# Kernel tuning notes

Measured on AMD Instinct MI355X. Metric: run time of the kernel, lower is better.

## Reference

```python
import jax, jax.numpy as jnp
import numpy as np

N = 100_000   # nodes
E = 1_600_000 # edges (avg degree 16)
D = 128       # input_dim
H = 128       # hidden_dim
G = 64        # graphs in batch
C = 2         # num_classes


def setup_inputs() -> dict:
    key = jax.random.key(0)
    ks = jax.random.split(key, 16)
    x = jax.random.normal(ks[0], (N, D), dtype=jnp.float32)
    edge_index = jax.random.randint(ks[1], (2, E), 0, N, dtype=jnp.int32)
    batch = jnp.sort(jax.random.randint(ks[2], (N,), 0, G, dtype=jnp.int32))
    def lin(k, fin, fout):
        s = 1.0 / np.sqrt(fin)
        kw, kb = jax.random.split(k)
        W = jax.random.uniform(kw, (fin, fout), jnp.float32, -s, s)
        b = jax.random.uniform(kb, (fout,), jnp.float32, -s, s)
        return W, b
    W0, b0 = lin(ks[3], D, H)
    W1, b1 = lin(ks[4], H, H)
    W2, b2 = lin(ks[5], H, H)
    Wc1, bc1 = lin(ks[6], 2 * H, H)
    Wc2, bc2 = lin(ks[7], H, C)
    return dict(x=x, edge_index=edge_index, batch=batch,
                W0=W0, b0=b0, W1=W1, b1=b1, W2=W2, b2=b2,
                Wc1=Wc1, bc1=bc1, Wc2=Wc2, bc2=bc2)


def _gcn_layer(x, W, b, src, dst, dinv):
    # GCNConv with self-loops and symmetric normalization:
    # out_i = sum_{j->i} d_j^{-1/2} d_i^{-1/2} (x_j W) + d_i^{-1} (x_i W) + b
    h = x @ W                                   # [N, H]
    coef = dinv[src] * dinv[dst]                # [E]
    agg = jax.ops.segment_sum(h[src] * coef[:, None], dst, num_segments=N)
    return agg + h * (dinv * dinv)[:, None] + b


def reference(x, edge_index, batch, W0, b0, W1, b1, W2, b2, Wc1, bc1, Wc2, bc2):
    src, dst = edge_index[0], edge_index[1]
    # degree with self-loops (in-degree on target nodes + 1)
    deg = jax.ops.segment_sum(jnp.ones((E,), jnp.float32), dst, num_segments=N) + 1.0
    dinv = jax.lax.rsqrt(deg)
    for W, b in ((W0, b0), (W1, b1), (W2, b2)):
        x = jax.nn.relu(_gcn_layer(x, W, b, src, dst, dinv))
        # dropout: inference mode -> identity
    # global mean pool per graph
    sums = jax.ops.segment_sum(x, batch, num_segments=G)            # [G, H]
    cnt = jax.ops.segment_sum(jnp.ones((N,), jnp.float32), batch, num_segments=G)
    pooled = sums / jnp.maximum(cnt, 1.0)[:, None]
    combined = jnp.concatenate([pooled, pooled], axis=1)            # [G, 2H]
    hcls = jax.nn.relu(combined @ Wc1 + bc1)
    return hcls @ Wc2 + bc2                                         # [G, C]
```

## Files before the change

kernel.cpp:

```cpp
#include <hip/hip_runtime.h>

#define HDIM 128
#define GCOUNT 64
#define CHUNK 2048

__device__ __forceinline__ float bfl(unsigned u) { return __uint_as_float(u << 16); }
__device__ __forceinline__ float bfh(unsigned u) { return __uint_as_float(u & 0xffff0000u); }
__device__ __forceinline__ unsigned short f2bf(float f) {
  unsigned u = __float_as_uint(f);
  unsigned r = (u + 0x7fffu + ((u >> 16) & 1u)) >> 16;
  return (unsigned short)r;
}
__device__ __forceinline__ unsigned pk2(float a, float b) {
  return (unsigned)f2bf(a) | ((unsigned)f2bf(b) << 16);
}

typedef __attribute__((ext_vector_type(8))) short short8;
typedef __attribute__((ext_vector_type(4))) float f32x4;

__device__ __forceinline__ unsigned qb(float v, float rinv) {
  int q = (int)rintf(v * rinv);
  return (unsigned)(q & 0xff);
}


__global__ void mega1(const float* __restrict__ W0, const float* __restrict__ W1,
                      const float* __restrict__ W2,
                      unsigned short* __restrict__ h0, unsigned short* __restrict__ l0,
                      unsigned short* __restrict__ h1, unsigned short* __restrict__ l1,
                      unsigned short* __restrict__ h2, unsigned short* __restrict__ l2,
                      float* __restrict__ pooled, float* __restrict__ gcnt, int pz,
                      const int* __restrict__ dst, int E, int G, int NB1,
                      int* __restrict__ gcount,
                      const float* __restrict__ x, uint2* __restrict__ S,
                      float* __restrict__ cs_base, int n) {
  __shared__ int hist[512];
  int b = blockIdx.x, t = threadIdx.x;
  if (b < 192) {
    int w = b >> 6;
    int idx = (b & 63) * 256 + t;
    const float* W = (w == 0) ? W0 : (w == 1) ? W1 : W2;
    unsigned short* hi = (w == 0) ? h0 : (w == 1) ? h1 : h2;
    unsigned short* lo = (w == 0) ? l0 : (w == 1) ? l1 : l2;
    int k = idx >> 7, nn = idx & 127;
    float wv = W[idx];
    unsigned short h = f2bf(wv);
    float hf = __uint_as_float((unsigned)h << 16);
    unsigned short l = f2bf(wv - hf);
    int kb = k >> 5, quad = (k >> 3) & 3, e = k & 7;
    int nt = nn >> 4, m = nn & 15;
    int di = (((kb * 8 + nt) * 64) + quad * 16 + m) * 8 + e;
    hi[di] = h;
    lo[di] = l;
  } else if (b < 192 + pz) {
    int i = (b - 192) * 256 + t;
    if (i < GCOUNT * HDIM) pooled[i] = 0.f;
    else if (i - GCOUNT * HDIM < GCOUNT) gcnt[i - GCOUNT * HDIM] = 0.f;
  } else if (b < 192 + pz + G) {
    int blk = b - 192 - pz;
    for (int i = t; i < NB1; i += 256) hist[i] = 0;
    __syncthreads();
    int base = blk * CHUNK;
    #pragma unroll
    for (int j = 0; j < CHUNK / 256; j++) {
      int e = base + j * 256 + t;
      if (e < E) atomicAdd(&hist[dst[e] >> 8], 1);
    }
    __syncthreads();
    for (int i = t; i < NB1; i += 256) gcount[i * G + blk] = hist[i];
  } else {
    int idx = (b - 192 - pz - G) * 16 + (t >> 4);
    int l = t & 15;
    int ridx = min(idx, n - 1);
    float4 f0 = ((const float4*)x)[(size_t)ridx * 32 + l * 2];
    float4 f1 = ((const float4*)x)[(size_t)ridx * 32 + l * 2 + 1];
    float v0 = f0.x, v1 = f0.y, v2 = f0.z, v3 = f0.w;
    float v4 = f1.x, v5 = f1.y, v6 = f1.z, v7 = f1.w;
    float mx = fmaxf(fmaxf(fmaxf(fabsf(v0), fabsf(v1)), fmaxf(fabsf(v2), fabsf(v3))),
                     fmaxf(fmaxf(fabsf(v4), fabsf(v5)), fmaxf(fabsf(v6), fabsf(v7))));
    mx = fmaxf(mx, __shfl_xor(mx, 1));
    mx = fmaxf(mx, __shfl_xor(mx, 2));
    mx = fmaxf(mx, __shfl_xor(mx, 4));
    mx = fmaxf(mx, __shfl_xor(mx, 8));
    float c = mx * (1.0f / 127.0f);
    float rinv = (mx > 0.f) ? 127.0f / mx : 0.f;
    if (idx < n) {
      unsigned lo = qb(v0, rinv) | (qb(v1, rinv) << 8) | (qb(v2, rinv) << 16) | (qb(v3, rinv) << 24);
      unsigned hi = qb(v4, rinv) | (qb(v5, rinv) << 8) | (qb(v6, rinv) << 16) | (qb(v7, rinv) << 24);
      S[(size_t)idx * 16 + l] = make_uint2(lo, hi);
      if (l == 0) cs_base[idx] = c;
    }
  }
}


__global__ void scanA(int* __restrict__ g, int* __restrict__ bsum, int M) {
  __shared__ int sh[1024];
  int t = threadIdx.x;
  int i = blockIdx.x * 1024 + t;
  int v = (i < M) ? g[i] : 0;
  sh[t] = v;
  __syncthreads();
  for (int off = 1; off < 1024; off <<= 1) {
    int u = (t >= off) ? sh[t - off] : 0;
    __syncthreads();
    sh[t] += u;
    __syncthreads();
  }
  if (i < M) g[i] = sh[t] - v;
  if (t == 1023) bsum[blockIdx.x] = sh[1023];
}

__global__ void scanB(int* __restrict__ g, const int* __restrict__ bsum, int nb, int M) {
  __shared__ int sh[512];
  int t = threadIdx.x;
  if (t < 512) sh[t] = (t < nb) ? bsum[t] : 0;
  __syncthreads();
  for (int off = 1; off < 512; off <<= 1) {
    int u = (t < 512 && t >= off) ? sh[t - off] : 0;
    __syncthreads();
    if (t < 512) sh[t] += u;
    __syncthreads();
  }
  #pragma unroll
  for (int k = 0; k < 2; k++) {
    int i = blockIdx.x * 2048 + k * 1024 + t;
    if (i < M) {
      int j = i >> 10;
      if (j) g[i] += sh[j - 1];
    }
  }
}


__global__ void rs_scatter(const int* __restrict__ src, const int* __restrict__ dst,
                           const int* __restrict__ gscan, int E, int G, int NB1,
                           uint2* __restrict__ sp) {
  __shared__ int run[512];
  int blk = blockIdx.x, t = threadIdx.x;
  for (int i = t; i < NB1; i += 256) run[i] = gscan[i * G + blk];
  __syncthreads();
  int base = blk * CHUNK;
  #pragma unroll
  for (int j = 0; j < CHUNK / 256; j++) {
    int e = base + j * 256 + t;
    if (e < E) {
      int d = dst[e];
      int pos = atomicAdd(&run[d >> 8], 1);
      sp[pos] = make_uint2((unsigned)d, (unsigned)src[e]);
    }
  }
}


__global__ void csr_fine(const uint2* __restrict__ sp, const int* __restrict__ gscan,
                         int E, int G, int NB1,
                         int* __restrict__ rowp, int* __restrict__ colv,
                         float* __restrict__ dinv, const float* __restrict__ cs_base,
                         float* __restrict__ cs, int n) {
  __shared__ int hist[256];
  __shared__ int scn[256];
  __shared__ int run2[256];
  int hb = blockIdx.x, t = threadIdx.x;
  int O = gscan[hb * G];
  int Oe = (hb == NB1 - 1) ? E : gscan[(hb + 1) * G];
  if (t < 256) hist[t] = 0;
  __syncthreads();
  for (int e = O + t; e < Oe; e += 512) atomicAdd(&hist[sp[e].x & 255], 1);
  __syncthreads();
  int v = 0;
  if (t < 256) { v = hist[t]; scn[t] = v; }
  __syncthreads();
  for (int off = 1; off < 256; off <<= 1) {
    int u = (t < 256 && t >= off) ? scn[t - off] : 0;
    __syncthreads();
    if (t < 256) scn[t] += u;
    __syncthreads();
  }
  if (t < 256) {
    int excl = scn[t] - v;
    run2[t] = O + excl;
    int d = (hb << 8) + t;
    rowp[d] = O + excl;
    if (d < n) {
      float dv = rsqrtf((float)v + 1.0f);
      dinv[d] = dv;
      cs[d] = cs_base[d] * dv;
    }
  }
  if (hb == NB1 - 1 && t == 0) rowp[n] = E;
  __syncthreads();
  for (int e = O + t; e < Oe; e += 512) {
    uint2 p = sp[e];
    int pos = atomicAdd(&run2[p.x & 255], 1);
    colv[pos] = (int)p.y;
  }
}


__device__ __forceinline__ void acc8(uint2 v, float c, float* a) {
  int xx = (int)v.x, yy = (int)v.y;
  a[0] += c * (float)(signed char)(xx);
  a[1] += c * (float)(signed char)(xx >> 8);
  a[2] += c * (float)(signed char)(xx >> 16);
  a[3] += c * (float)(xx >> 24);
  a[4] += c * (float)(signed char)(yy);
  a[5] += c * (float)(signed char)(yy >> 8);
  a[6] += c * (float)(signed char)(yy >> 16);
  a[7] += c * (float)(yy >> 24);
}


__device__ __forceinline__ void agg_phase(
    const uint2* __restrict__ S, const float* __restrict__ cs,
    const float* __restrict__ dinv,
    const int* __restrict__ rowp, const int* __restrict__ col,
    uint4* At, int block0, int t, int n) {
  int grp = t >> 4, gl = t & 15;
  #pragma unroll 1
  for (int k = 0; k < 4; k++) {
    int lrow = grp * 4 + k;
    int g = block0 + lrow;
    uint4 o = make_uint4(0u, 0u, 0u, 0u);
    if (g < n) {
      float a[8];
      {
        uint2 q = S[(size_t)g * 16 + gl];
        float c = cs[g];
        int xx = (int)q.x, yy = (int)q.y;
        a[0] = c * (float)(signed char)(xx);
        a[1] = c * (float)(signed char)(xx >> 8);
        a[2] = c * (float)(signed char)(xx >> 16);
        a[3] = c * (float)(xx >> 24);
        a[4] = c * (float)(signed char)(yy);
        a[5] = c * (float)(signed char)(yy >> 8);
        a[6] = c * (float)(signed char)(yy >> 16);
        a[7] = c * (float)(yy >> 24);
      }
      int e0 = rowp[g], e1 = rowp[g + 1];
      int e = e0;
      for (; e + 7 < e1; e += 8) {
        int s0 = col[e],     s1 = col[e + 1], s2 = col[e + 2], s3 = col[e + 3];
        int s4 = col[e + 4], s5 = col[e + 5], s6 = col[e + 6], s7 = col[e + 7];
        uint2 q0 = S[(size_t)s0 * 16 + gl];
        uint2 q1 = S[(size_t)s1 * 16 + gl];
        uint2 q2 = S[(size_t)s2 * 16 + gl];
        uint2 q3 = S[(size_t)s3 * 16 + gl];
        uint2 q4 = S[(size_t)s4 * 16 + gl];
        uint2 q5 = S[(size_t)s5 * 16 + gl];
        uint2 q6 = S[(size_t)s6 * 16 + gl];
        uint2 q7 = S[(size_t)s7 * 16 + gl];
        float c0 = cs[s0], c1 = cs[s1], c2 = cs[s2], c3 = cs[s3];
        float c4 = cs[s4], c5 = cs[s5], c6 = cs[s6], c7 = cs[s7];
        acc8(q0, c0, a); acc8(q1, c1, a); acc8(q2, c2, a); acc8(q3, c3, a);
        acc8(q4, c4, a); acc8(q5, c5, a); acc8(q6, c6, a); acc8(q7, c7, a);
      }
      for (; e + 3 < e1; e += 4) {
        int s0 = col[e], s1 = col[e + 1], s2 = col[e + 2], s3 = col[e + 3];
        uint2 q0 = S[(size_t)s0 * 16 + gl];
        uint2 q1 = S[(size_t)s1 * 16 + gl];
        uint2 q2 = S[(size_t)s2 * 16 + gl];
        uint2 q3 = S[(size_t)s3 * 16 + gl];
        float c0 = cs[s0], c1 = cs[s1], c2 = cs[s2], c3 = cs[s3];
        acc8(q0, c0, a); acc8(q1, c1, a); acc8(q2, c2, a); acc8(q3, c3, a);
      }
      for (; e < e1; e++) {
        int s = col[e];
        uint2 q = S[(size_t)s * 16 + gl];
        acc8(q, cs[s], a);
      }
      float d = dinv[g];
      o.x = pk2(a[0] * d, a[1] * d);
      o.y = pk2(a[2] * d, a[3] * d);
      o.z = pk2(a[4] * d, a[5] * d);
      o.w = pk2(a[6] * d, a[7] * d);
    }
    At[(gl << 6) + (lrow ^ (gl & 7))] = o;
  }
}

__device__ __forceinline__ void stage16(uint4* Wl, const uint4* __restrict__ WT, int t) {
  #pragma unroll
  for (int i = 0; i < 4; i++) {
    int idx = t + i * 256;
    Wl[idx] = WT[idx];
  }
}

__device__ __forceinline__ void mfma2(const uint4* Wl, const uint4* av, f32x4* acc,
                                      int kbase, int lane) {
  #pragma unroll
  for (int kk = 0; kk < 2; kk++) {
    short8 af = __builtin_bit_cast(short8, av[kbase + kk]);
    #pragma unroll
    for (int nt = 0; nt < 8; nt++) {
      uint4 b = Wl[(kk * 8 + nt) * 64 + lane];
      acc[nt] = __builtin_amdgcn_mfma_f32_16x16x32_bf16(af, __builtin_bit_cast(short8, b), acc[nt], 0, 0, 0);
    }
  }
}

__global__ __launch_bounds__(256, 8) void fused_q8(
    const uint2* __restrict__ S, const float* __restrict__ cs,
    const float* __restrict__ dinv,
    const int* __restrict__ rowp, const int* __restrict__ col,
    const uint4* __restrict__ WThi, const uint4* __restrict__ WTlo,
    const float* __restrict__ bias,
    unsigned char* __restrict__ Sout, float* __restrict__ csout, int n) {
  __shared__ __align__(16) char smem[16384];
  uint4* At = (uint4*)smem;
  uint4* Wl = (uint4*)smem;
  int t = threadIdx.x;
  int lane = t & 63, wv = t >> 6;
  int m = lane & 15, quad = lane >> 4;
  int block0 = blockIdx.x * 64;

  agg_phase(S, cs, dinv, rowp, col, At, block0, t, n);
  __syncthreads();

  uint4 av[4];
  #pragma unroll
  for (int kb = 0; kb < 4; kb++) {
    int glr = kb * 4 + quad;
    av[kb] = At[(glr << 6) + ((wv * 16 + m) ^ (glr & 7))];
  }
  __syncthreads();

  f32x4 acc[8];
  #pragma unroll
  for (int i = 0; i < 8; i++) acc[i] = (f32x4){0.f, 0.f, 0.f, 0.f};

  stage16(Wl, WThi, t);        __syncthreads();
  mfma2(Wl, av, acc, 0, lane); __syncthreads();
  stage16(Wl, WThi + 1024, t); __syncthreads();
  mfma2(Wl, av, acc, 2, lane); __syncthreads();
  stage16(Wl, WTlo, t);        __syncthreads();
  mfma2(Wl, av, acc, 0, lane); __syncthreads();
  stage16(Wl, WTlo + 1024, t); __syncthreads();
  mfma2(Wl, av, acc, 2, lane); __syncthreads();

  char* stg = smem;
  float* LcA = (float*)(smem + 9216);
  #pragma unroll
  for (int r = 0; r < 4; r++) {
    int lrow = wv * 16 + quad * 4 + r;
    int grow = block0 + lrow;
    float sc = (grow < n) ? dinv[grow] : 0.f;
    float v[8];
    float mx = 0.f;
    #pragma unroll
    for (int nt = 0; nt < 8; nt++) {
      v[nt] = fmaxf(acc[nt][r] + bias[nt * 16 + m], 0.f) * sc;
      mx = fmaxf(mx, v[nt]);
    }
    mx = fmaxf(mx, __shfl_xor(mx, 1));
    mx = fmaxf(mx, __shfl_xor(mx, 2));
    mx = fmaxf(mx, __shfl_xor(mx, 4));
    mx = fmaxf(mx, __shfl_xor(mx, 8));
    float c = mx * (1.0f / 127.0f);
    float rinv = (mx > 0.f) ? 127.0f / mx : 0.f;
    #pragma unroll
    for (int nt = 0; nt < 8; nt++) {
      stg[lrow * 144 + nt * 16 + m] = (char)(int)rintf(v[nt] * rinv);
    }
    if (m == 0) LcA[lrow] = c;
  }
  __syncthreads();
  for (int i = t; i < 512; i += 256) {
    int lrow = i >> 3, seg = i & 7;
    int grow = block0 + lrow;
    if (grow < n)
      ((uint4*)Sout)[(size_t)grow * 8 + seg] = *(const uint4*)&stg[lrow * 144 + seg * 16];
  }
  if (t < 64 && block0 + t < n) csout[block0 + t] = LcA[t];
}

__global__ __launch_bounds__(256, 8) void fused_final(
    const uint2* __restrict__ S, const float* __restrict__ cs,
    const float* __restrict__ dinv,
    const int* __restrict__ rowp, const int* __restrict__ col,
    const uint4* __restrict__ WThi, const uint4* __restrict__ WTlo,
    const float* __restrict__ bias, const int* __restrict__ batch,
    float* __restrict__ pooled, float* __restrict__ gcnt, int n) {
  __shared__ __align__(16) char smem[16384];
  uint4* At = (uint4*)smem;
  uint4* Wl = (uint4*)smem;
  int t = threadIdx.x;
  int lane = t & 63, wv = t >> 6;
  int m = lane & 15, quad = lane >> 4;
  int block0 = blockIdx.x * 64;

  agg_phase(S, cs, dinv, rowp, col, At, block0, t, n);
  __syncthreads();

  uint4 av[4];
  #pragma unroll
  for (int kb = 0; kb < 4; kb++) {
    int glr = kb * 4 + quad;
    av[kb] = At[(glr << 6) + ((wv * 16 + m) ^ (glr & 7))];
  }
  __syncthreads();

  f32x4 acc[8];
  #pragma unroll
  for (int i = 0; i < 8; i++) acc[i] = (f32x4){0.f, 0.f, 0.f, 0.f};

  stage16(Wl, WThi, t);        __syncthreads();
  mfma2(Wl, av, acc, 0, lane); __syncthreads();
  stage16(Wl, WThi + 1024, t); __syncthreads();
  mfma2(Wl, av, acc, 2, lane); __syncthreads();
  stage16(Wl, WTlo, t);        __syncthreads();
  mfma2(Wl, av, acc, 0, lane); __syncthreads();
  stage16(Wl, WTlo + 1024, t); __syncthreads();
  mfma2(Wl, av, acc, 2, lane); __syncthreads();

  unsigned short* Ls = (unsigned short*)smem;
  #pragma unroll
  for (int r = 0; r < 4; r++) {
    int lrow = wv * 16 + quad * 4 + r;
    #pragma unroll
    for (int nt = 0; nt < 8; nt++) {
      float v = fmaxf(acc[nt][r] + bias[nt * 16 + m], 0.f);
      Ls[lrow * 128 + nt * 16 + m] = f2bf(v);
    }
  }
  __syncthreads();
  if (t < 128) {
    float a2 = 0.f, cl = 0.f;
    int gcur = -1;
    for (int r = 0; r < 64; r++) {
      int grow = block0 + r;
      if (grow >= n) break;
      int gr = batch[grow];
      if (gr != gcur) {
        if (gcur >= 0) {
          atomicAdd(&pooled[gcur * HDIM + t], a2);
          if (t == 0) atomicAdd(&gcnt[gcur], cl);
        }
        a2 = 0.f; cl = 0.f; gcur = gr;
      }
      a2 += bfl((unsigned)Ls[r * 128 + t]);
      cl += 1.f;
    }
    if (gcur >= 0) {
      atomicAdd(&pooled[gcur * HDIM + t], a2);
      if (t == 0) atomicAdd(&gcnt[gcur], cl);
    }
  }
}


__global__ void cls_kernel(const float* __restrict__ pooled, const float* __restrict__ gcnt,
                           const float* __restrict__ Wc1, const float* __restrict__ bc1,
                           const float* __restrict__ Wc2, const float* __restrict__ bc2,
                           float* __restrict__ out) {
  __shared__ float p[HDIM];
  __shared__ float r0s[HDIM], r1s[HDIM];
  int g = blockIdx.x, t = threadIdx.x;
  float c = fmaxf(gcnt[g], 1.0f);
  p[t] = pooled[g * HDIM + t] / c;
  __syncthreads();
  float acc = bc1[t];
  for (int k = 0; k < HDIM; k++) {
    acc += p[k] * (Wc1[k * HDIM + t] + Wc1[(HDIM + k) * HDIM + t]);
  }
  float h = fmaxf(acc, 0.f);
  r0s[t] = h * Wc2[t * 2 + 0];
  r1s[t] = h * Wc2[t * 2 + 1];
  __syncthreads();
  for (int s2 = 64; s2 > 0; s2 >>= 1) {
    if (t < s2) { r0s[t] += r0s[t + s2]; r1s[t] += r1s[t + s2]; }
    __syncthreads();
  }
  if (t == 0) {
    out[g * 2 + 0] = r0s[0] + bc2[0];
    out[g * 2 + 1] = r1s[0] + bc2[1];
  }
}


extern "C" void kernel_launch(void* const* d_in, const int* in_sizes, int n_in,
                              void* d_out, int out_size, void* d_ws, size_t ws_size,
                              hipStream_t stream) {
  const float* x   = (const float*)d_in[0];
  const int*   ei  = (const int*)d_in[1];
  const int*   bat = (const int*)d_in[2];
  const float* W0  = (const float*)d_in[3];
  const float* b0  = (const float*)d_in[4];
  const float* W1  = (const float*)d_in[5];
  const float* b1  = (const float*)d_in[6];
  const float* W2  = (const float*)d_in[7];
  const float* b2  = (const float*)d_in[8];
  const float* Wc1 = (const float*)d_in[9];
  const float* bc1 = (const float*)d_in[10];
  const float* Wc2 = (const float*)d_in[11];
  const float* bc2 = (const float*)d_in[12];
  float* out = (float*)d_out;

  int N = in_sizes[0] / HDIM;
  int E = in_sizes[1] / 2;
  const int* src = ei;
  const int* dst = ei + E;

  int NB1 = (N + 255) >> 8;
  int G = (E + CHUNK - 1) / CHUNK;
  int M = NB1 * G;

  char* ws = (char*)d_ws;
  size_t off = 0;
  auto alloc = [&](size_t bytes) -> void* {
    void* p = (void*)(ws + off);
    off += (bytes + 511) & ~(size_t)511;
    return p;
  };
  unsigned char* Sa = (unsigned char*)alloc((size_t)N * HDIM * 2);
  unsigned char* Sb = Sa + (size_t)N * HDIM;
  float* csa  = (float*)alloc((size_t)N * 4);
  float* csb  = (float*)alloc((size_t)N * 4);
  float* cs_base = (float*)alloc((size_t)N * 4);
  float* dinv = (float*)alloc((size_t)N * 4);
  int*   rowp = (int*)alloc((size_t)(NB1 * 256 + 2) * 4);
  int*   colv = (int*)alloc((size_t)E * 4);
  uint2* sp   = (uint2*)alloc((size_t)E * 8);
  float* pooled = (float*)alloc((size_t)GCOUNT * HDIM * 4);
  float* gcnt   = (float*)alloc((size_t)GCOUNT * 4);
  unsigned short* wt_hi[3], *wt_lo[3];
  for (int i = 0; i < 3; i++) {
    wt_hi[i] = (unsigned short*)alloc(HDIM * HDIM * 2);
    wt_lo[i] = (unsigned short*)alloc(HDIM * HDIM * 2);
  }
  int* gcount = (int*)alloc((size_t)(M + 2) * 4);
  int nbM = (M + 1023) / 1024;
  int* bsum = (int*)alloc((size_t)nbM * 4);

  int pz = (GCOUNT * HDIM + GCOUNT + 255) / 256;
  int psb = (N + 15) / 16;
  mega1<<<192 + pz + G + psb, 256, 0, stream>>>(W0, W1, W2,
      wt_hi[0], wt_lo[0], wt_hi[1], wt_lo[1], wt_hi[2], wt_lo[2],
      pooled, gcnt, pz, dst, E, G, NB1, gcount,
      x, (uint2*)Sa, cs_base, N);

  scanA<<<nbM, 1024, 0, stream>>>(gcount, bsum, M);
  scanB<<<(M + 2047) / 2048, 1024, 0, stream>>>(gcount, bsum, nbM, M);

  rs_scatter<<<G, 256, 0, stream>>>(src, dst, gcount, E, G, NB1, sp);
  csr_fine<<<NB1, 512, 0, stream>>>(sp, gcount, E, G, NB1, rowp, colv,
      dinv, cs_base, csa, N);

  int fusedBlocks = (N + 63) / 64;

  fused_q8<<<fusedBlocks, 256, 0, stream>>>((const uint2*)Sa, csa, dinv, rowp, colv,
      (const uint4*)wt_hi[0], (const uint4*)wt_lo[0], b0, Sb, csb, N);

  fused_q8<<<fusedBlocks, 256, 0, stream>>>((const uint2*)Sb, csb, dinv, rowp, colv,
      (const uint4*)wt_hi[1], (const uint4*)wt_lo[1], b1, Sa, csa, N);

  fused_final<<<fusedBlocks, 256, 0, stream>>>((const uint2*)Sa, csa, dinv, rowp, colv,
      (const uint4*)wt_hi[2], (const uint4*)wt_lo[2], b2, bat, pooled, gcnt, N);

  cls_kernel<<<GCOUNT, HDIM, 0, stream>>>(pooled, gcnt, Wc1, bc1, Wc2, bc2, out);
}
```

Before: 342.3 us.

## Pad CSR rows to multiples of four and make fused layers wave-local

Each CSR row is padded to a multiple of four, with pad entries pointing at a zeroed dummy node N, so the aggregation can use int4 column loads and needs no scalar tail loop. Each wave now aggregates and multiplies its own 16 rows in a private LDS slice, using wave-level fences instead of block-wide barriers. The bf16 hi/lo weights are read straight from global memory (through cache) instead of being staged in LDS. This trades the block barriers and staging for redundant per-wave weight loads, extra colv and rowe memory, and up to three padded gathers per row.

```diff
diff --git a/kernel.cpp b/kernel.cpp
--- a/kernel.cpp
+++ b/kernel.cpp
@@ -5,7 +5,6 @@
 #define CHUNK 2048
 
 __device__ __forceinline__ float bfl(unsigned u) { return __uint_as_float(u << 16); }
-__device__ __forceinline__ float bfh(unsigned u) { return __uint_as_float(u & 0xffff0000u); }
 __device__ __forceinline__ unsigned short f2bf(float f) {
   unsigned u = __float_as_uint(f);
   unsigned r = (u + 0x7fffu + ((u >> 16) & 1u)) >> 16;
@@ -21,6 +20,12 @@
 __device__ __forceinline__ unsigned qb(float v, float rinv) {
   int q = (int)rintf(v * rinv);
   return (unsigned)(q & 0xff);
+}
+
+__device__ __forceinline__ void wave_lds_fence() {
+  __builtin_amdgcn_wave_barrier();
+  asm volatile("s_waitcnt lgkmcnt(0)" ::: "memory");
+  __builtin_amdgcn_sched_barrier(0);
 }
 
 
@@ -33,6 +38,8 @@
                       const int* __restrict__ dst, int E, int G, int NB1,
                       int* __restrict__ gcount,
                       const float* __restrict__ x, uint2* __restrict__ S,
+                      uint2* __restrict__ Sb, float* __restrict__ csaP,
+                      float* __restrict__ csbP,
                       float* __restrict__ cs_base, int n) {
   __shared__ int hist[512];
   int b = blockIdx.x, t = threadIdx.x;
@@ -56,6 +63,12 @@
     int i = (b - 192) * 256 + t;
     if (i < GCOUNT * HDIM) pooled[i] = 0.f;
     else if (i - GCOUNT * HDIM < GCOUNT) gcnt[i - GCOUNT * HDIM] = 0.f;
+    if (b == 192) {
+      if (t < 16) S[(size_t)n * 16 + t] = make_uint2(0u, 0u);
+      else if (t < 32) Sb[(size_t)n * 16 + (t - 16)] = make_uint2(0u, 0u);
+      else if (t == 32) csaP[n] = 0.f;
+      else if (t == 33) csbP[n] = 0.f;
+    }
   } else if (b < 192 + pz + G) {
     int blk = b - 192 - pz;
     for (int i = t; i < NB1; i += 256) hist[i] = 0;
@@ -155,7 +168,8 @@
 
 __global__ void csr_fine(const uint2* __restrict__ sp, const int* __restrict__ gscan,
                          int E, int G, int NB1,
-                         int* __restrict__ rowp, int* __restrict__ colv,
+                         int* __restrict__ rowp, int* __restrict__ rowe,
+                         int* __restrict__ colv,
                          float* __restrict__ dinv, const float* __restrict__ cs_base,
                          float* __restrict__ cs, int n) {
   __shared__ int hist[256];
@@ -164,12 +178,13 @@
   int hb = blockIdx.x, t = threadIdx.x;
   int O = gscan[hb * G];
   int Oe = (hb == NB1 - 1) ? E : gscan[(hb + 1) * G];
+  int PO = ((O + 3) & ~3) + hb * 1024;
   if (t < 256) hist[t] = 0;
   __syncthreads();
   for (int e = O + t; e < Oe; e += 512) atomicAdd(&hist[sp[e].x & 255], 1);
   __syncthreads();
-  int v = 0;
-  if (t < 256) { v = hist[t]; scn[t] = v; }
+  int v = 0, pv = 0;
+  if (t < 256) { v = hist[t]; pv = (v + 3) & ~3; scn[t] = pv; }
   __syncthreads();
   for (int off = 1; off < 256; off <<= 1) {
     int u = (t < 256 && t >= off) ? scn[t - off] : 0;
@@ -178,17 +193,18 @@
     __syncthreads();
   }
   if (t < 256) {
-    int excl = scn[t] - v;
-    run2[t] = O + excl;
+    int st = PO + scn[t] - pv;
+    run2[t] = st;
     int d = (hb << 8) + t;
-    rowp[d] = O + excl;
+    rowp[d] = st;
+    rowe[d] = st + pv;
+    for (int i = v; i < pv; i++) colv[st + i] = n;
     if (d < n) {
       float dv = rsqrtf((float)v + 1.0f);
       dinv[d] = dv;
       cs[d] = cs_base[d] * dv;
     }
   }
-  if (hb == NB1 - 1 && t == 0) rowp[n] = E;
   __syncthreads();
   for (int e = O + t; e < Oe; e += 512) {
     uint2 p = sp[e];
@@ -211,16 +227,17 @@
 }
 
 
-__device__ __forceinline__ void agg_phase(
+__device__ __forceinline__ void agg_wave(
     const uint2* __restrict__ S, const float* __restrict__ cs,
     const float* __restrict__ dinv,
-    const int* __restrict__ rowp, const int* __restrict__ col,
-    uint4* At, int block0, int t, int n) {
-  int grp = t >> 4, gl = t & 15;
+    const int* __restrict__ rowp, const int* __restrict__ rowe,
+    const int* __restrict__ col,
+    uint4* Atw, int row0, int lane, int n) {
+  int j = lane >> 4, gl = lane & 15;
   #pragma unroll 1
   for (int k = 0; k < 4; k++) {
-    int lrow = grp * 4 + k;
-    int g = block0 + lrow;
+    int r = j * 4 + k;
+    int g = row0 + r;
     uint4 o = make_uint4(0u, 0u, 0u, 0u);
     if (g < n) {
       float a[8];
@@ -237,37 +254,31 @@
         a[6] = c * (float)(signed char)(yy >> 16);
         a[7] = c * (float)(yy >> 24);
       }
-      int e0 = rowp[g], e1 = rowp[g + 1];
-      int e = e0;
+      int e = rowp[g], e1 = rowe[g];
       for (; e + 7 < e1; e += 8) {
-        int s0 = col[e],     s1 = col[e + 1], s2 = col[e + 2], s3 = col[e + 3];
-        int s4 = col[e + 4], s5 = col[e + 5], s6 = col[e + 6], s7 = col[e + 7];
-        uint2 q0 = S[(size_t)s0 * 16 + gl];
-        uint2 q1 = S[(size_t)s1 * 16 + gl];
-        uint2 q2 = S[(size_t)s2 * 16 + gl];
-        uint2 q3 = S[(size_t)s3 * 16 + gl];
-        uint2 q4 = S[(size_t)s4 * 16 + gl];
-        uint2 q5 = S[(size_t)s5 * 16 + gl];
-        uint2 q6 = S[(size_t)s6 * 16 + gl];
-        uint2 q7 = S[(size_t)s7 * 16 + gl];
-        float c0 = cs[s0], c1 = cs[s1], c2 = cs[s2], c3 = cs[s3];
-        float c4 = cs[s4], c5 = cs[s5], c6 = cs[s6], c7 = cs[s7];
+        int4 ca = *(const int4*)(col + e);
+        int4 cb = *(const int4*)(col + e + 4);
+        uint2 q0 = S[(size_t)ca.x * 16 + gl];
+        uint2 q1 = S[(size_t)ca.y * 16 + gl];
+        uint2 q2 = S[(size_t)ca.z * 16 + gl];
+        uint2 q3 = S[(size_t)ca.w * 16 + gl];
+        uint2 q4 = S[(size_t)cb.x * 16 + gl];
+        uint2 q5 = S[(size_t)cb.y * 16 + gl];
+        uint2 q6 = S[(size_t)cb.z * 16 + gl];
+        uint2 q7 = S[(size_t)cb.w * 16 + gl];
+        float c0 = cs[ca.x], c1 = cs[ca.y], c2 = cs[ca.z], c3 = cs[ca.w];
+        float c4 = cs[cb.x], c5 = cs[cb.y], c6 = cs[cb.z], c7 = cs[cb.w];
         acc8(q0, c0, a); acc8(q1, c1, a); acc8(q2, c2, a); acc8(q3, c3, a);
         acc8(q4, c4, a); acc8(q5, c5, a); acc8(q6, c6, a); acc8(q7, c7, a);
       }
-      for (; e + 3 < e1; e += 4) {
-        int s0 = col[e], s1 = col[e + 1], s2 = col[e + 2], s3 = col[e + 3];
-        uint2 q0 = S[(size_t)s0 * 16 + gl];
-        uint2 q1 = S[(size_t)s1 * 16 + gl];
-        uint2 q2 = S[(size_t)s2 * 16 + gl];
-        uint2 q3 = S[(size_t)s3 * 16 + gl];
-        float c0 = cs[s0], c1 = cs[s1], c2 = cs[s2], c3 = cs[s3];
+      if (e < e1) {
+        int4 ca = *(const int4*)(col + e);
+        uint2 q0 = S[(size_t)ca.x * 16 + gl];
+        uint2 q1 = S[(size_t)ca.y * 16 + gl];
+        uint2 q2 = S[(size_t)ca.z * 16 + gl];
+        uint2 q3 = S[(size_t)ca.w * 16 + gl];
+        float c0 = cs[ca.x], c1 = cs[ca.y], c2 = cs[ca.z], c3 = cs[ca.w];
         acc8(q0, c0, a); acc8(q1, c1, a); acc8(q2, c2, a); acc8(q3, c3, a);
-      }
-      for (; e < e1; e++) {
-        int s = col[e];
-        uint2 q = S[(size_t)s * 16 + gl];
-        acc8(q, cs[s], a);
       }
       float d = dinv[g];
       o.x = pk2(a[0] * d, a[1] * d);
@@ -275,26 +286,31 @@
       o.z = pk2(a[4] * d, a[5] * d);
       o.w = pk2(a[6] * d, a[7] * d);
     }
-    At[(gl << 6) + (lrow ^ (gl & 7))] = o;
-  }
-}
-
-__device__ __forceinline__ void stage16(uint4* Wl, const uint4* __restrict__ WT, int t) {
-  #pragma unroll
-  for (int i = 0; i < 4; i++) {
-    int idx = t + i * 256;
-    Wl[idx] = WT[idx];
-  }
-}
-
-__device__ __forceinline__ void mfma2(const uint4* Wl, const uint4* av, f32x4* acc,
-                                      int kbase, int lane) {
-  #pragma unroll
-  for (int kk = 0; kk < 2; kk++) {
-    short8 af = __builtin_bit_cast(short8, av[kbase + kk]);
+    Atw[(gl << 4) + (r ^ (gl & 7))] = o;
+  }
+}
+
+__device__ __forceinline__ void gemm_wave(const uint4* av,
+                                          const uint4* __restrict__ WThi,
+                                          const uint4* __restrict__ WTlo,
+                                          f32x4* acc, int lane) {
+  #pragma unroll
+  for (int kb = 0; kb < 4; kb++) {
+    short8 af = __builtin_bit_cast(short8, av[kb]);
+    const uint4* wp = WThi + (kb * 8) * 64 + lane;
     #pragma unroll
     for (int nt = 0; nt < 8; nt++) {
-      uint4 b = Wl[(kk * 8 + nt) * 64 + lane];
+      uint4 b = wp[nt * 64];
+      acc[nt] = __builtin_amdgcn_mfma_f32_16x16x32_bf16(af, __builtin_bit_cast(short8, b), acc[nt], 0, 0, 0);
+    }
+  }
+  #pragma unroll
+  for (int kb = 0; kb < 4; kb++) {
+    short8 af = __builtin_bit_cast(short8, av[kb]);
+    const uint4* wp = WTlo + (kb * 8) * 64 + lane;
+    #pragma unroll
+    for (int nt = 0; nt < 8; nt++) {
+      uint4 b = wp[nt * 64];
       acc[nt] = __builtin_amdgcn_mfma_f32_16x16x32_bf16(af, __builtin_bit_cast(short8, b), acc[nt], 0, 0, 0);
     }
   }
@@ -303,48 +319,40 @@
 __global__ __launch_bounds__(256, 8) void fused_q8(
     const uint2* __restrict__ S, const float* __restrict__ cs,
     const float* __restrict__ dinv,
-    const int* __restrict__ rowp, const int* __restrict__ col,
+    const int* __restrict__ rowp, const int* __restrict__ rowe,
+    const int* __restrict__ col,
     const uint4* __restrict__ WThi, const uint4* __restrict__ WTlo,
     const float* __restrict__ bias,
     unsigned char* __restrict__ Sout, float* __restrict__ csout, int n) {
   __shared__ __align__(16) char smem[16384];
-  uint4* At = (uint4*)smem;
-  uint4* Wl = (uint4*)smem;
   int t = threadIdx.x;
   int lane = t & 63, wv = t >> 6;
   int m = lane & 15, quad = lane >> 4;
-  int block0 = blockIdx.x * 64;
-
-  agg_phase(S, cs, dinv, rowp, col, At, block0, t, n);
-  __syncthreads();
+  int row0 = blockIdx.x * 64 + wv * 16;
+  uint4* Atw = (uint4*)(smem + (wv << 12));
+
+  agg_wave(S, cs, dinv, rowp, rowe, col, Atw, row0, lane, n);
+  wave_lds_fence();
 
   uint4 av[4];
   #pragma unroll
   for (int kb = 0; kb < 4; kb++) {
     int glr = kb * 4 + quad;
-    av[kb] = At[(glr << 6) + ((wv * 16 + m) ^ (glr & 7))];
-  }
-  __syncthreads();
+    av[kb] = Atw[(glr << 4) + (m ^ (glr & 7))];
+  }
 
   f32x4 acc[8];
   #pragma unroll
   for (int i = 0; i < 8; i++) acc[i] = (f32x4){0.f, 0.f, 0.f, 0.f};
-
-  stage16(Wl, WThi, t);        __syncthreads();
-  mfma2(Wl, av, acc, 0, lane); __syncthreads();
-  stage16(Wl, WThi + 1024, t); __syncthreads();
-  mfma2(Wl, av, acc, 2, lane); __syncthreads();
-  stage16(Wl, WTlo, t);        __syncthreads();
-  mfma2(Wl, av, acc, 0, lane); __syncthreads();
-  stage16(Wl, WTlo + 1024, t); __syncthreads();
-  mfma2(Wl, av, acc, 2, lane); __syncthreads();
-
-  char* stg = smem;
-  float* LcA = (float*)(smem + 9216);
+  gemm_wave(av, WThi, WTlo, acc, lane);
+
+  char* stg = (char*)Atw;
+  float* Lc = (float*)(stg + 2304);
+  __builtin_amdgcn_wave_barrier();
   #pragma unroll
   for (int r = 0; r < 4; r++) {
-    int lrow = wv * 16 + quad * 4 + r;
-    int grow = block0 + lrow;
+    int wrow = quad * 4 + r;
+    int grow = row0 + wrow;
     float sc = (grow < n) ? dinv[grow] : 0.f;
     float v[8];
     float mx = 0.f;
@@ -361,59 +369,54 @@
     float rinv = (mx > 0.f) ? 127.0f / mx : 0.f;
     #pragma unroll
     for (int nt = 0; nt < 8; nt++) {
-      stg[lrow * 144 + nt * 16 + m] = (char)(int)rintf(v[nt] * rinv);
-    }
-    if (m == 0) LcA[lrow] = c;
-  }
-  __syncthreads();
-  for (int i = t; i < 512; i += 256) {
-    int lrow = i >> 3, seg = i & 7;
-    int grow = block0 + lrow;
+      stg[wrow * 144 + nt * 16 + m] = (char)(int)rintf(v[nt] * rinv);
+    }
+    if (m == 0) Lc[wrow] = c;
+  }
+  wave_lds_fence();
+  #pragma unroll
+  for (int z = 0; z < 2; z++) {
+    int i = lane + z * 64;
+    int wrow = i >> 3, seg = i & 7;
+    int grow = row0 + wrow;
     if (grow < n)
-      ((uint4*)Sout)[(size_t)grow * 8 + seg] = *(const uint4*)&stg[lrow * 144 + seg * 16];
-  }
-  if (t < 64 && block0 + t < n) csout[block0 + t] = LcA[t];
+      ((uint4*)Sout)[(size_t)grow * 8 + seg] = *(const uint4*)&stg[wrow * 144 + seg * 16];
+  }
+  if (lane < 16 && row0 + lane < n) csout[row0 + lane] = Lc[lane];
 }
 
 __global__ __launch_bounds__(256, 8) void fused_final(
     const uint2* __restrict__ S, const float* __restrict__ cs,
     const float* __restrict__ dinv,
-    const int* __restrict__ rowp, const int* __restrict__ col,
+    const int* __restrict__ rowp, const int* __restrict__ rowe,
+    const int* __restrict__ col,
     const uint4* __restrict__ WThi, const uint4* __restrict__ WTlo,
     const float* __restrict__ bias, const int* __restrict__ batch,
     float* __restrict__ pooled, float* __restrict__ gcnt, int n) {
   __shared__ __align__(16) char smem[16384];
-  uint4* At = (uint4*)smem;
-  uint4* Wl = (uint4*)smem;
   int t = threadIdx.x;
   int lane = t & 63, wv = t >> 6;
   int m = lane & 15, quad = lane >> 4;
   int block0 = blockIdx.x * 64;
-
-  agg_phase(S, cs, dinv, rowp, col, At, block0, t, n);
-  __syncthreads();
+  int row0 = block0 + wv * 16;
+  uint4* Atw = (uint4*)(smem + (wv << 12));
+
+  agg_wave(S, cs, dinv, rowp, rowe, col, Atw, row0, lane, n);
+  wave_lds_fence();
 
   uint4 av[4];
   #pragma unroll
   for (int kb = 0; kb < 4; kb++) {
     int glr = kb * 4 + quad;
-    av[kb] = At[(glr << 6) + ((wv * 16 + m) ^ (glr & 7))];
-  }
-  __syncthreads();
+    av[kb] = Atw[(glr << 4) + (m ^ (glr & 7))];
+  }
 
   f32x4 acc[8];
   #pragma unroll
   for (int i = 0; i < 8; i++) acc[i] = (f32x4){0.f, 0.f, 0.f, 0.f};
-
-  stage16(Wl, WThi, t);        __syncthreads();
-  mfma2(Wl, av, acc, 0, lane); __syncthreads();
-  stage16(Wl, WThi + 1024, t); __syncthreads();
-  mfma2(Wl, av, acc, 2, lane); __syncthreads();
-  stage16(Wl, WTlo, t);        __syncthreads();
-  mfma2(Wl, av, acc, 0, lane); __syncthreads();
-  stage16(Wl, WTlo + 1024, t); __syncthreads();
-  mfma2(Wl, av, acc, 2, lane); __syncthreads();
-
+  gemm_wave(av, WThi, WTlo, acc, lane);
+
+  __syncthreads();
   unsigned short* Ls = (unsigned short*)smem;
   #pragma unroll
   for (int r = 0; r < 4; r++) {
@@ -513,14 +516,15 @@
     off += (bytes + 511) & ~(size_t)511;
     return p;
   };
-  unsigned char* Sa = (unsigned char*)alloc((size_t)N * HDIM * 2);
-  unsigned char* Sb = Sa + (size_t)N * HDIM;
-  float* csa  = (float*)alloc((size_t)N * 4);
-  float* csb  = (float*)alloc((size_t)N * 4);
+  unsigned char* Sa = (unsigned char*)alloc((size_t)(N + 1) * HDIM * 2);
+  unsigned char* Sb = Sa + (size_t)(N + 1) * HDIM;
+  float* csa  = (float*)alloc((size_t)(N + 2) * 4);
+  float* csb  = (float*)alloc((size_t)(N + 2) * 4);
   float* cs_base = (float*)alloc((size_t)N * 4);
   float* dinv = (float*)alloc((size_t)N * 4);
   int*   rowp = (int*)alloc((size_t)(NB1 * 256 + 2) * 4);
-  int*   colv = (int*)alloc((size_t)E * 4);
+  int*   rowe = (int*)alloc((size_t)(NB1 * 256 + 2) * 4);
+  int*   colv = (int*)alloc((size_t)(E + NB1 * 1024 + 1024) * 4);
   uint2* sp   = (uint2*)alloc((size_t)E * 8);
   float* pooled = (float*)alloc((size_t)GCOUNT * HDIM * 4);
   float* gcnt   = (float*)alloc((size_t)GCOUNT * 4);
@@ -538,24 +542,24 @@
   mega1<<<192 + pz + G + psb, 256, 0, stream>>>(W0, W1, W2,
       wt_hi[0], wt_lo[0], wt_hi[1], wt_lo[1], wt_hi[2], wt_lo[2],
       pooled, gcnt, pz, dst, E, G, NB1, gcount,
-      x, (uint2*)Sa, cs_base, N);
+      x, (uint2*)Sa, (uint2*)Sb, csa, csb, cs_base, N);
 
   scanA<<<nbM, 1024, 0, stream>>>(gcount, bsum, M);
   scanB<<<(M + 2047) / 2048, 1024, 0, stream>>>(gcount, bsum, nbM, M);
 
   rs_scatter<<<G, 256, 0, stream>>>(src, dst, gcount, E, G, NB1, sp);
-  csr_fine<<<NB1, 512, 0, stream>>>(sp, gcount, E, G, NB1, rowp, colv,
+  csr_fine<<<NB1, 512, 0, stream>>>(sp, gcount, E, G, NB1, rowp, rowe, colv,
       dinv, cs_base, csa, N);
 
   int fusedBlocks = (N + 63) / 64;
 
-  fused_q8<<<fusedBlocks, 256, 0, stream>>>((const uint2*)Sa, csa, dinv, rowp, colv,
+  fused_q8<<<fusedBlocks, 256, 0, stream>>>((const uint2*)Sa, csa, dinv, rowp, rowe, colv,
       (const uint4*)wt_hi[0], (const uint4*)wt_lo[0], b0, Sb, csb, N);
 
-  fused_q8<<<fusedBlocks, 256, 0, stream>>>((const uint2*)Sb, csb, dinv, rowp, colv,
+  fused_q8<<<fusedBlocks, 256, 0, stream>>>((const uint2*)Sb, csb, dinv, rowp, rowe, colv,
       (const uint4*)wt_hi[1], (const uint4*)wt_lo[1], b1, Sa, csa, N);
 
-  fused_final<<<fusedBlocks, 256, 0, stream>>>((const uint2*)Sa, csa, dinv, rowp, colv,
+  fused_final<<<fusedBlocks, 256, 0, stream>>>((const uint2*)Sa, csa, dinv, rowp, rowe, colv,
       (const uint4*)wt_hi[2], (const uint4*)wt_lo[2], b2, bat, pooled, gcnt, N);
 
   cls_kernel<<<GCOUNT, HDIM, 0, stream>>>(pooled, gcnt, Wc1, bc1, Wc2, bc2, out);
```

After: 389.4 us. 13.8% more time.

## Pad CSR rows to multiples of four with a zero sentinel node for vectorized gather

Applied to the files above, without the earlier changes.

Each CSR row is padded to a multiple of four entries, filled with a sentinel node index n whose feature row and scale are zeroed. Rows get separate start and end arrays with 16-byte-aligned starts. The aggregation loop can then load column indices as int4 with a one-step prefetch and needs no tail loops. The launch-bounds occupancy hint is also relaxed from 8 to 4, giving the compiler more registers. In exchange, every padded slot costs an extra gather of the zero row, and the serial per-thread padding fill adds some work to CSR construction.

```diff
diff --git a/kernel.cpp b/kernel.cpp
--- a/kernel.cpp
+++ b/kernel.cpp
@@ -5,7 +5,6 @@
 #define CHUNK 2048
 
 __device__ __forceinline__ float bfl(unsigned u) { return __uint_as_float(u << 16); }
-__device__ __forceinline__ float bfh(unsigned u) { return __uint_as_float(u & 0xffff0000u); }
 __device__ __forceinline__ unsigned short f2bf(float f) {
   unsigned u = __float_as_uint(f);
   unsigned r = (u + 0x7fffu + ((u >> 16) & 1u)) >> 16;
@@ -33,6 +32,8 @@
                       const int* __restrict__ dst, int E, int G, int NB1,
                       int* __restrict__ gcount,
                       const float* __restrict__ x, uint2* __restrict__ S,
+                      uint2* __restrict__ Sb, float* __restrict__ csaP,
+                      float* __restrict__ csbP,
                       float* __restrict__ cs_base, int n) {
   __shared__ int hist[512];
   int b = blockIdx.x, t = threadIdx.x;
@@ -56,6 +57,12 @@
     int i = (b - 192) * 256 + t;
     if (i < GCOUNT * HDIM) pooled[i] = 0.f;
     else if (i - GCOUNT * HDIM < GCOUNT) gcnt[i - GCOUNT * HDIM] = 0.f;
+    if (b == 192) {
+      if (t < 16) S[(size_t)n * 16 + t] = make_uint2(0u, 0u);
+      else if (t < 32) Sb[(size_t)n * 16 + (t - 16)] = make_uint2(0u, 0u);
+      else if (t == 32) csaP[n] = 0.f;
+      else if (t == 33) csbP[n] = 0.f;
+    }
   } else if (b < 192 + pz + G) {
     int blk = b - 192 - pz;
     for (int i = t; i < NB1; i += 256) hist[i] = 0;
@@ -155,7 +162,8 @@
 
 __global__ void csr_fine(const uint2* __restrict__ sp, const int* __restrict__ gscan,
                          int E, int G, int NB1,
-                         int* __restrict__ rowp, int* __restrict__ colv,
+                         int* __restrict__ rowp, int* __restrict__ rowe,
+                         int* __restrict__ colv,
                          float* __restrict__ dinv, const float* __restrict__ cs_base,
                          float* __restrict__ cs, int n) {
   __shared__ int hist[256];
@@ -164,12 +172,13 @@
   int hb = blockIdx.x, t = threadIdx.x;
   int O = gscan[hb * G];
   int Oe = (hb == NB1 - 1) ? E : gscan[(hb + 1) * G];
+  int PO = ((O + 3) & ~3) + hb * 1024;
   if (t < 256) hist[t] = 0;
   __syncthreads();
   for (int e = O + t; e < Oe; e += 512) atomicAdd(&hist[sp[e].x & 255], 1);
   __syncthreads();
-  int v = 0;
-  if (t < 256) { v = hist[t]; scn[t] = v; }
+  int v = 0, pv = 0;
+  if (t < 256) { v = hist[t]; pv = (v + 3) & ~3; scn[t] = pv; }
   __syncthreads();
   for (int off = 1; off < 256; off <<= 1) {
     int u = (t < 256 && t >= off) ? scn[t - off] : 0;
@@ -178,17 +187,18 @@
     __syncthreads();
   }
   if (t < 256) {
-    int excl = scn[t] - v;
-    run2[t] = O + excl;
+    int st = PO + scn[t] - pv;
+    run2[t] = st;
     int d = (hb << 8) + t;
-    rowp[d] = O + excl;
+    rowp[d] = st;
+    rowe[d] = st + pv;
+    for (int i = v; i < pv; i++) colv[st + i] = n;
     if (d < n) {
       float dv = rsqrtf((float)v + 1.0f);
       dinv[d] = dv;
       cs[d] = cs_base[d] * dv;
     }
   }
-  if (hb == NB1 - 1 && t == 0) rowp[n] = E;
   __syncthreads();
   for (int e = O + t; e < Oe; e += 512) {
     uint2 p = sp[e];
@@ -214,7 +224,8 @@
 __device__ __forceinline__ void agg_phase(
     const uint2* __restrict__ S, const float* __restrict__ cs,
     const float* __restrict__ dinv,
-    const int* __restrict__ rowp, const int* __restrict__ col,
+    const int* __restrict__ rowp, const int* __restrict__ rowe,
+    const int* __restrict__ col,
     uint4* At, int block0, int t, int n) {
   int grp = t >> 4, gl = t & 15;
   #pragma unroll 1
@@ -237,37 +248,26 @@
         a[6] = c * (float)(signed char)(yy >> 16);
         a[7] = c * (float)(yy >> 24);
       }
-      int e0 = rowp[g], e1 = rowp[g + 1];
-      int e = e0;
-      for (; e + 7 < e1; e += 8) {
-        int s0 = col[e],     s1 = col[e + 1], s2 = col[e + 2], s3 = col[e + 3];
-        int s4 = col[e + 4], s5 = col[e + 5], s6 = col[e + 6], s7 = col[e + 7];
-        uint2 q0 = S[(size_t)s0 * 16 + gl];
-        uint2 q1 = S[(size_t)s1 * 16 + gl];
-        uint2 q2 = S[(size_t)s2 * 16 + gl];
-        uint2 q3 = S[(size_t)s3 * 16 + gl];
-        uint2 q4 = S[(size_t)s4 * 16 + gl];
-        uint2 q5 = S[(size_t)s5 * 16 + gl];
-        uint2 q6 = S[(size_t)s6 * 16 + gl];
-        uint2 q7 = S[(size_t)s7 * 16 + gl];
-        float c0 = cs[s0], c1 = cs[s1], c2 = cs[s2], c3 = cs[s3];
-        float c4 = cs[s4], c5 = cs[s5], c6 = cs[s6], c7 = cs[s7];
+      int e = rowp[g], e1 = rowe[g];
+      if (e < e1) {
+        int4 ca = *(const int4*)(col + e);
+        #pragma unroll 1
+        for (e += 4; e < e1; e += 4) {
+          int4 cn = *(const int4*)(col + e);
+          uint2 q0 = S[(size_t)ca.x * 16 + gl];
+          uint2 q1 = S[(size_t)ca.y * 16 + gl];
+          uint2 q2 = S[(size_t)ca.z * 16 + gl];
+          uint2 q3 = S[(size_t)ca.w * 16 + gl];
+          float c0 = cs[ca.x], c1 = cs[ca.y], c2 = cs[ca.z], c3 = cs[ca.w];
+          acc8(q0, c0, a); acc8(q1, c1, a); acc8(q2, c2, a); acc8(q3, c3, a);
+          ca = cn;
+        }
+        uint2 q0 = S[(size_t)ca.x * 16 + gl];
+        uint2 q1 = S[(size_t)ca.y * 16 + gl];
+        uint2 q2 = S[(size_t)ca.z * 16 + gl];
+        uint2 q3 = S[(size_t)ca.w * 16 + gl];
+        float c0 = cs[ca.x], c1 = cs[ca.y], c2 = cs[ca.z], c3 = cs[ca.w];
         acc8(q0, c0, a); acc8(q1, c1, a); acc8(q2, c2, a); acc8(q3, c3, a);
-        acc8(q4, c4, a); acc8(q5, c5, a); acc8(q6, c6, a); acc8(q7, c7, a);
-      }
-      for (; e + 3 < e1; e += 4) {
-        int s0 = col[e], s1 = col[e + 1], s2 = col[e + 2], s3 = col[e + 3];
-        uint2 q0 = S[(size_t)s0 * 16 + gl];
-        uint2 q1 = S[(size_t)s1 * 16 + gl];
-        uint2 q2 = S[(size_t)s2 * 16 + gl];
-        uint2 q3 = S[(size_t)s3 * 16 + gl];
-        float c0 = cs[s0], c1 = cs[s1], c2 = cs[s2], c3 = cs[s3];
-        acc8(q0, c0, a); acc8(q1, c1, a); acc8(q2, c2, a); acc8(q3, c3, a);
-      }
-      for (; e < e1; e++) {
-        int s = col[e];
-        uint2 q = S[(size_t)s * 16 + gl];
-        acc8(q, cs[s], a);
       }
       float d = dinv[g];
       o.x = pk2(a[0] * d, a[1] * d);
@@ -300,10 +300,11 @@
   }
 }
 
-__global__ __launch_bounds__(256, 8) void fused_q8(
+__global__ __launch_bounds__(256, 4) void fused_q8(
     const uint2* __restrict__ S, const float* __restrict__ cs,
     const float* __restrict__ dinv,
-    const int* __restrict__ rowp, const int* __restrict__ col,
+    const int* __restrict__ rowp, const int* __restrict__ rowe,
+    const int* __restrict__ col,
     const uint4* __restrict__ WThi, const uint4* __restrict__ WTlo,
     const float* __restrict__ bias,
     unsigned char* __restrict__ Sout, float* __restrict__ csout, int n) {
@@ -315,7 +316,7 @@
   int m = lane & 15, quad = lane >> 4;
   int block0 = blockIdx.x * 64;
 
-  agg_phase(S, cs, dinv, rowp, col, At, block0, t, n);
+  agg_phase(S, cs, dinv, rowp, rowe, col, At, block0, t, n);
   __syncthreads();
 
   uint4 av[4];
@@ -375,10 +376,11 @@
   if (t < 64 && block0 + t < n) csout[block0 + t] = LcA[t];
 }
 
-__global__ __launch_bounds__(256, 8) void fused_final(
+__global__ __launch_bounds__(256, 4) void fused_final(
     const uint2* __restrict__ S, const float* __restrict__ cs,
     const float* __restrict__ dinv,
-    const int* __restrict__ rowp, const int* __restrict__ col,
+    const int* __restrict__ rowp, const int* __restrict__ rowe,
+    const int* __restrict__ col,
     const uint4* __restrict__ WThi, const uint4* __restrict__ WTlo,
     const float* __restrict__ bias, const int* __restrict__ batch,
     float* __restrict__ pooled, float* __restrict__ gcnt, int n) {
@@ -390,7 +392,7 @@
   int m = lane & 15, quad = lane >> 4;
   int block0 = blockIdx.x * 64;
 
-  agg_phase(S, cs, dinv, rowp, col, At, block0, t, n);
+  agg_phase(S, cs, dinv, rowp, rowe, col, At, block0, t, n);
   __syncthreads();
 
   uint4 av[4];
@@ -513,14 +515,15 @@
     off += (bytes + 511) & ~(size_t)511;
     return p;
   };
-  unsigned char* Sa = (unsigned char*)alloc((size_t)N * HDIM * 2);
-  unsigned char* Sb = Sa + (size_t)N * HDIM;
-  float* csa  = (float*)alloc((size_t)N * 4);
-  float* csb  = (float*)alloc((size_t)N * 4);
+  unsigned char* Sa = (unsigned char*)alloc((size_t)(N + 1) * HDIM * 2);
+  unsigned char* Sb = Sa + (size_t)(N + 1) * HDIM;
+  float* csa  = (float*)alloc((size_t)(N + 2) * 4);
+  float* csb  = (float*)alloc((size_t)(N + 2) * 4);
   float* cs_base = (float*)alloc((size_t)N * 4);
   float* dinv = (float*)alloc((size_t)N * 4);
   int*   rowp = (int*)alloc((size_t)(NB1 * 256 + 2) * 4);
-  int*   colv = (int*)alloc((size_t)E * 4);
+  int*   rowe = (int*)alloc((size_t)(NB1 * 256 + 2) * 4);
+  int*   colv = (int*)alloc((size_t)(E + NB1 * 1024 + 1024) * 4);
   uint2* sp   = (uint2*)alloc((size_t)E * 8);
   float* pooled = (float*)alloc((size_t)GCOUNT * HDIM * 4);
   float* gcnt   = (float*)alloc((size_t)GCOUNT * 4);
@@ -538,24 +541,24 @@
   mega1<<<192 + pz + G + psb, 256, 0, stream>>>(W0, W1, W2,
       wt_hi[0], wt_lo[0], wt_hi[1], wt_lo[1], wt_hi[2], wt_lo[2],
       pooled, gcnt, pz, dst, E, G, NB1, gcount,
-      x, (uint2*)Sa, cs_base, N);
+      x, (uint2*)Sa, (uint2*)Sb, csa, csb, cs_base, N);
 
   scanA<<<nbM, 1024, 0, stream>>>(gcount, bsum, M);
   scanB<<<(M + 2047) / 2048, 1024, 0, stream>>>(gcount, bsum, nbM, M);
 
   rs_scatter<<<G, 256, 0, stream>>>(src, dst, gcount, E, G, NB1, sp);
-  csr_fine<<<NB1, 512, 0, stream>>>(sp, gcount, E, G, NB1, rowp, colv,
+  csr_fine<<<NB1, 512, 0, stream>>>(sp, gcount, E, G, NB1, rowp, rowe, colv,
       dinv, cs_base, csa, N);
 
   int fusedBlocks = (N + 63) / 64;
 
-  fused_q8<<<fusedBlocks, 256, 0, stream>>>((const uint2*)Sa, csa, dinv, rowp, colv,
+  fused_q8<<<fusedBlocks, 256, 0, stream>>>((const uint2*)Sa, csa, dinv, rowp, rowe, colv,
       (const uint4*)wt_hi[0], (const uint4*)wt_lo[0], b0, Sb, csb, N);
 
-  fused_q8<<<fusedBlocks, 256, 0, stream>>>((const uint2*)Sb, csb, dinv, rowp, colv,
+  fused_q8<<<fusedBlocks, 256, 0, stream>>>((const uint2*)Sb, csb, dinv, rowp, rowe, colv,
       (const uint4*)wt_hi[1], (const uint4*)wt_lo[1], b1, Sa, csa, N);
 
-  fused_final<<<fusedBlocks, 256, 0, stream>>>((const uint2*)Sa, csa, dinv, rowp, colv,
+  fused_final<<<fusedBlocks, 256, 0, stream>>>((const uint2*)Sa, csa, dinv, rowp, rowe, colv,
       (const uint4*)wt_hi[2], (const uint4*)wt_lo[2], b2, bat, pooled, gcnt, N);
 
   cls_kernel<<<GCOUNT, HDIM, 0, stream>>>(pooled, gcnt, Wc1, bc1, Wc2, bc2, out);
```

After: 330.5 us. 3.5% less time.
